# Performance work log

Measured on AMD Instinct MI355X. Metric: run time of the kernel, lower is better.

Reference implementation:

```python
import jax, jax.numpy as jnp
import numpy as np

TOP_K = 2


def setup_inputs() -> dict:
    key = jax.random.key(0)
    k1, k2, k3, k4 = jax.random.split(key, 4)
    B, S, H, I, E = 8, 2048, 768, 3072, 8
    x = jax.random.normal(k1, (B, S, H), dtype=jnp.float32)
    # kaiming_uniform-ish scale for weights
    router_w = jax.random.uniform(k2, (E, H), dtype=jnp.float32, minval=-1.0, maxval=1.0) * (1.0 / np.sqrt(H))
    up_w = jax.random.uniform(k3, (E, H, I), dtype=jnp.float32, minval=-1.0, maxval=1.0) * (1.0 / np.sqrt(H))
    down_w = jax.random.uniform(k4, (E, I, H), dtype=jnp.float32, minval=-1.0, maxval=1.0) * (1.0 / np.sqrt(I))
    return {"x": x, "router_w": router_w, "up_w": up_w, "down_w": down_w}


def reference(x, router_w, up_w, down_w):
    B, S, H = x.shape
    E = up_w.shape[0]
    T = B * S
    xf = x.reshape(T, H)
    # router: Linear(H -> E, bias=False) then softmax, top-k, renormalize
    logits = xf @ router_w.T                      # [T, E]
    probs = jax.nn.softmax(logits, axis=-1)
    top_w, top_i = jax.lax.top_k(probs, TOP_K)    # [T, K]
    top_w = top_w / jnp.sum(top_w, axis=-1, keepdims=True)
    # dense per-(token, expert) gate: zero for unselected experts
    gate = jnp.zeros((T, E), dtype=xf.dtype).at[jnp.arange(T)[:, None], top_i].add(top_w)
    # combine: sum_e gate[:, e] * down_e(gelu(up_e(x)))
    out = jnp.zeros_like(xf)
    for e in range(E):  # fixed small expert count; loop is structural, not over data dims
        h = jax.nn.gelu(xf @ up_w[e], approximate=False)   # exact GELU == torch F.gelu
        out = out + gate[:, e:e + 1] * (h @ down_w[e])
    return out.reshape(B, S, H)
```

## Files before the change

### kernel.cpp

```cpp
#include <hip/hip_runtime.h>

typedef short bf16x8 __attribute__((ext_vector_type(8)));
typedef float f32x4  __attribute__((ext_vector_type(4)));

#define T_TOK 16384
#define HD 768
#define ID 3072
#define NE 8

__device__ __forceinline__ unsigned short f2bf(float f) {
    unsigned int u = __float_as_uint(f);
    unsigned int r = (u + 0x7FFFu + ((u >> 16) & 1u)) >> 16;
    return (unsigned short)r;
}

__device__ __forceinline__ void gload16(const void* g, void* l) {
    __builtin_amdgcn_global_load_lds(
        (const __attribute__((address_space(1))) void*)g,
        (__attribute__((address_space(3))) void*)l, 16, 0, 0);
}

__global__ __launch_bounds__(256) void k_cvt_x(const float* __restrict__ x,
                                               unsigned short* __restrict__ xb) {
    int i = blockIdx.x * 256 + threadIdx.x;
    float4 v = ((const float4*)x)[i];
    ushort4 o;
    o.x = f2bf(v.x); o.y = f2bf(v.y); o.z = f2bf(v.z); o.w = f2bf(v.w);
    ((ushort4*)xb)[i] = o;
}

__global__ __launch_bounds__(256) void k_tp(const float* __restrict__ in,
                                            unsigned short* __restrict__ out,
                                            int R, int C) {
    __shared__ float t[64][65];
    const float* ine = in + (size_t)blockIdx.z * R * C;
    unsigned short* oute = out + (size_t)blockIdx.z * R * C;
    int c0 = blockIdx.x * 64, r0 = blockIdx.y * 64;
    int lc = threadIdx.x & 63, lr4 = threadIdx.x >> 6;
#pragma unroll
    for (int i = 0; i < 16; i++) {
        int r = i * 4 + lr4;
        t[r][lc] = ine[(size_t)(r0 + r) * C + c0 + lc];
    }
    __syncthreads();
#pragma unroll
    for (int i = 0; i < 16; i++) {
        int r = i * 4 + lr4;
        oute[(size_t)(c0 + r) * R + r0 + lc] = f2bf(t[lc][r]);
    }
}

__global__ __launch_bounds__(256) void k_router(const float* __restrict__ x,
                                                const float* __restrict__ rw,
                                                int* __restrict__ topE,
                                                float* __restrict__ topW) {
    __shared__ float lrw[NE * HD];
    for (int i = threadIdx.x; i < NE * HD; i += 256) lrw[i] = rw[i];
    __syncthreads();
    int lane = threadIdx.x & 63;
    int t = blockIdx.x * 4 + (threadIdx.x >> 6);
    const float* xr = x + (size_t)t * HD;
    float acc[NE] = {0, 0, 0, 0, 0, 0, 0, 0};
    for (int h = lane; h < HD; h += 64) {
        float xv = xr[h];
#pragma unroll
        for (int e = 0; e < NE; e++) acc[e] = fmaf(xv, lrw[e * HD + h], acc[e]);
    }
#pragma unroll
    for (int e = 0; e < NE; e++) {
        float v = acc[e];
#pragma unroll
        for (int o = 32; o > 0; o >>= 1) v += __shfl_xor(v, o, 64);
        acc[e] = v;
    }
    if (lane == 0) {
        int e1 = 0; float l1 = acc[0];
#pragma unroll
        for (int e = 1; e < NE; e++) if (acc[e] > l1) { l1 = acc[e]; e1 = e; }
        int e2 = -1; float l2 = -1e30f;
#pragma unroll
        for (int e = 0; e < NE; e++) if (e != e1 && acc[e] > l2) { l2 = acc[e]; e2 = e; }
        float ex = expf(l2 - l1);
        float w1 = 1.0f / (1.0f + ex);
        topE[2 * t] = e1; topE[2 * t + 1] = e2;
        topW[2 * t] = w1; topW[2 * t + 1] = ex * w1;
    }
}

__global__ __launch_bounds__(256) void k_scatter(const int* __restrict__ topE,
                                                 const float* __restrict__ topW,
                                                 int* __restrict__ counts,
                                                 int* __restrict__ tokL,
                                                 float* __restrict__ gateL) {
    __shared__ int lc[NE], lbase[NE];
    if (threadIdx.x < NE) lc[threadIdx.x] = 0;
    __syncthreads();
    int t = blockIdx.x * 256 + threadIdx.x;
    int e1 = topE[2 * t], e2 = topE[2 * t + 1];
    int p1 = atomicAdd(&lc[e1], 1);
    int p2 = atomicAdd(&lc[e2], 1);
    __syncthreads();
    if (threadIdx.x < NE) lbase[threadIdx.x] = atomicAdd(&counts[threadIdx.x], lc[threadIdx.x]);
    __syncthreads();
    int q1 = lbase[e1] + p1, q2 = lbase[e2] + p2;
    tokL[e1 * T_TOK + q1] = t;  gateL[e1 * T_TOK + q1] = topW[2 * t];
    tokL[e2 * T_TOK + q2] = t;  gateL[e2 * T_TOK + q2] = topW[2 * t + 1];
}

__global__ __launch_bounds__(512, 2) void k_moe(
    const unsigned short* __restrict__ xb,
    const unsigned short* __restrict__ upt,
    const unsigned short* __restrict__ dnt,
    const int* __restrict__ counts,
    const int* __restrict__ tokL,
    const float* __restrict__ gateL,
    float* __restrict__ out) {
    __shared__ __align__(16) char lds[155648];
    char* xs = lds;
    char* hs = lds + 98304;
    char* ring = lds + 106496;

    const int e = blockIdx.x & 7;
    const int slot = blockIdx.x >> 3;
    const int cnt = counts[e];
    if (slot * 64 >= cnt) return;
    const int nrow = min(64, cnt - slot * 64);
    const int* tok = tokL + e * T_TOK + slot * 64;
    const float* gat = gateL + e * T_TOK + slot * 64;

    const int tid = threadIdx.x;
    const int lane = tid & 63;
    const int wid = tid >> 6;
    const int mi = wid >> 2, ni = wid & 3;

    const char* upe = (const char*)(upt + (size_t)e * ID * HD);
    const char* dne = (const char*)(dnt + (size_t)e * HD * ID);

    {
        int off = tid * 16;
#pragma unroll
        for (int s = 0; s < 12; s++) {
            int o = off + s * 8192;
            int m = o / 1536;
            int cb = o - m * 1536;
            int tk = (m < nrow) ? tok[m] : tok[0];
            const char* src = (const char*)xb + (size_t)tk * 1536 + (size_t)(cb ^ ((m & 7) << 4));
            gload16(src, xs + s * 8192 + wid * 1024);
        }
    }
    asm volatile("s_waitcnt vmcnt(0)" ::: "memory");
    __builtin_amdgcn_s_barrier();
    asm volatile("" ::: "memory");

    auto issue = [&](int s) {
        char* dst = ring + (s % 6) * 8192 + wid * 1024;
        int ci = s / 24;
        int ph = s - ci * 24;
        int row = tid >> 3;
        int cb = (tid & 7) << 4;
        int scb = cb ^ ((row & 7) << 4);
        const char* src;
        if (ci >= 48) src = upe;
        else if (ph < 12) src = upe + (size_t)(ci * 64 + row) * 1536 + ph * 128 + scb;
        else              src = dne + (size_t)((ph - 12) * 64 + row) * 6144 + ci * 128 + scb;
        gload16(src, dst);
    };

    f32x4 acc[2][12];
#pragma unroll
    for (int a = 0; a < 2; a++)
#pragma unroll
        for (int b = 0; b < 12; b++) acc[a][b] = (f32x4){0.f, 0.f, 0.f, 0.f};

    issue(0); issue(1); issue(2); issue(3);

    f32x4 acch[2];
    bf16x8 ha[2][2];

    for (int ci = 0; ci < 48; ci++) {
#pragma unroll
        for (int ks = 0; ks < 12; ks++) {
            issue(ci * 24 + ks + 4);
            asm volatile("s_waitcnt vmcnt(4)" ::: "memory");
            __builtin_amdgcn_s_barrier();
            asm volatile("" ::: "memory");
            char* buf = ring + (ks % 6) * 8192;
            if (ks == 0) { acch[0] = (f32x4){0.f,0.f,0.f,0.f}; acch[1] = (f32x4){0.f,0.f,0.f,0.f}; }
#pragma unroll
            for (int kr = 0; kr < 2; kr++) {
                int bn = ni * 16 + (lane & 15);
                int bo = ((kr * 32 + (lane >> 4) * 8) * 2) ^ ((bn & 7) << 4);
                bf16x8 bfrag = *(const bf16x8*)(buf + bn * 128 + bo);
#pragma unroll
                for (int mr = 0; mr < 2; mr++) {
                    int ar = mi * 32 + mr * 16 + (lane & 15);
                    int ao = ((ks * 64 + kr * 32 + (lane >> 4) * 8) * 2) ^ ((ar & 7) << 4);
                    bf16x8 afrag = *(const bf16x8*)(xs + ar * 1536 + ao);
                    acch[mr] = __builtin_amdgcn_mfma_f32_16x16x32_bf16(afrag, bfrag, acch[mr], 0, 0, 0);
                }
            }
            if (ks == 11) {
#pragma unroll
                for (int mr = 0; mr < 2; mr++) {
                    int col = ni * 16 + (lane & 15);
#pragma unroll
                    for (int r = 0; r < 4; r++) {
                        int m = mi * 32 + mr * 16 + (lane >> 4) * 4 + r;
                        float v = acch[mr][r];
                        float g = 0.5f * v * (1.0f + erff(v * 0.70710678118f));
                        *(unsigned short*)(hs + m * 128 + ((col * 2) ^ ((m & 7) << 4))) = f2bf(g);
                    }
                }
                asm volatile("s_waitcnt lgkmcnt(0)" ::: "memory");
            }
        }
#pragma unroll
        for (int j = 0; j < 12; j++) {
            issue(ci * 24 + 12 + j + 4);
            asm volatile("s_waitcnt vmcnt(4)" ::: "memory");
            __builtin_amdgcn_s_barrier();
            asm volatile("" ::: "memory");
            char* buf = ring + ((12 + j) % 6) * 8192;
            if (j == 0) {
#pragma unroll
                for (int mr = 0; mr < 2; mr++)
#pragma unroll
                    for (int kr = 0; kr < 2; kr++) {
                        int ar = mi * 32 + mr * 16 + (lane & 15);
                        int ao = ((kr * 32 + (lane >> 4) * 8) * 2) ^ ((ar & 7) << 4);
                        ha[mr][kr] = *(const bf16x8*)(hs + ar * 128 + ao);
                    }
            }
#pragma unroll
            for (int kr = 0; kr < 2; kr++) {
                int bn = ni * 16 + (lane & 15);
                int bo = ((kr * 32 + (lane >> 4) * 8) * 2) ^ ((bn & 7) << 4);
                bf16x8 bfrag = *(const bf16x8*)(buf + bn * 128 + bo);
#pragma unroll
                for (int mr = 0; mr < 2; mr++)
                    acc[mr][j] = __builtin_amdgcn_mfma_f32_16x16x32_bf16(ha[mr][kr], bfrag, acc[mr][j], 0, 0, 0);
            }
        }
    }

    int   t4[2][4];
    float g4[2][4];
#pragma unroll
    for (int mr = 0; mr < 2; mr++)
#pragma unroll
        for (int r = 0; r < 4; r++) {
            int m = mi * 32 + mr * 16 + (lane >> 4) * 4 + r;
            bool valid = m < nrow;
            t4[mr][r] = valid ? tok[m] : -1;
            g4[mr][r] = valid ? gat[m] : 0.f;
        }
#pragma unroll
    for (int mr = 0; mr < 2; mr++)
#pragma unroll
        for (int j = 0; j < 12; j++) {
            int colg = j * 64 + ni * 16 + (lane & 15);
#pragma unroll
            for (int r = 0; r < 4; r++) {
                if (t4[mr][r] >= 0)
                    atomicAdd(out + (size_t)t4[mr][r] * HD + colg, g4[mr][r] * acc[mr][j][r]);
            }
        }
}

extern "C" void kernel_launch(void* const* d_in, const int* in_sizes, int n_in,
                              void* d_out, int out_size, void* d_ws, size_t ws_size,
                              hipStream_t stream) {
    const float* x  = (const float*)d_in[0];
    const float* rw = (const float*)d_in[1];
    const float* uw = (const float*)d_in[2];
    const float* dw = (const float*)d_in[3];
    float* out = (float*)d_out;

    char* w = (char*)d_ws;
    unsigned short* xb  = (unsigned short*)w; w += (size_t)T_TOK * HD * 2;
    unsigned short* upt = (unsigned short*)w; w += (size_t)NE * ID * HD * 2;
    unsigned short* dnt = (unsigned short*)w; w += (size_t)NE * HD * ID * 2;
    int*   topE   = (int*)w;   w += (size_t)T_TOK * 2 * 4;
    float* topW   = (float*)w; w += (size_t)T_TOK * 2 * 4;
    int*   counts = (int*)w;   w += 256;
    int*   tokL   = (int*)w;   w += (size_t)NE * T_TOK * 4;
    float* gateL  = (float*)w; w += (size_t)NE * T_TOK * 4;

    hipMemsetAsync(d_out, 0, (size_t)T_TOK * HD * 4, stream);
    hipMemsetAsync(counts, 0, 256, stream);

    k_cvt_x<<<(T_TOK * HD) / (256 * 4), 256, 0, stream>>>(x, xb);
    k_tp<<<dim3(ID / 64, HD / 64, NE), 256, 0, stream>>>(uw, upt, HD, ID);
    k_tp<<<dim3(HD / 64, ID / 64, NE), 256, 0, stream>>>(dw, dnt, ID, HD);
    k_router<<<T_TOK / 4, 256, 0, stream>>>(x, rw, topE, topW);
    k_scatter<<<T_TOK / 256, 256, 0, stream>>>(topE, topW, counts, tokL, gateL);
    k_moe<<<2048, 512, 0, stream>>>(xb, upt, dnt, counts, tokL, gateL, out);
}
```

Baseline: 779.4 us.

## Rewrite fused MoE kernel with compact tile list, register-held X and wider intermediate chunks

Replaces the MoE kernel with a new fused version. A small descriptor kernel builds a compact list of (expert, row-offset) tiles so no empty blocks are launched, and an XCD-aware swizzle maps blocks to tiles. The token activations are now held in registers instead of LDS. The intermediate dimension is processed in 128-wide chunks, with a 3-slot ring for up-projection weights and double-buffered down-projection slices. The up-projection and the down-projection loads are interleaved, and s_setprio is raised around MFMA bursts. Exact erff is swapped for a polynomial erf approximation. The 24 f32x4 down accumulators plus 24 held activation fragments raise register pressure, and the polynomial slightly changes GELU accuracy.

```diff
diff --git a/kernel.cpp b/kernel.cpp
--- a/kernel.cpp
+++ b/kernel.cpp
@@ -7,6 +7,7 @@
 #define HD 768
 #define ID 3072
 #define NE 8
+#define NTM64 520
 
 __device__ __forceinline__ unsigned short f2bf(float f) {
     unsigned int u = __float_as_uint(f);
@@ -18,6 +19,29 @@
     __builtin_amdgcn_global_load_lds(
         (const __attribute__((address_space(1))) void*)g,
         (__attribute__((address_space(3))) void*)l, 16, 0, 0);
+}
+
+__device__ __forceinline__ void vmw(int n) {
+    if (n == 0)      asm volatile("s_waitcnt vmcnt(0)" ::: "memory");
+    else if (n == 2) asm volatile("s_waitcnt vmcnt(2)" ::: "memory");
+    else if (n == 3) asm volatile("s_waitcnt vmcnt(3)" ::: "memory");
+    else             asm volatile("s_waitcnt vmcnt(4)" ::: "memory");
+}
+
+__device__ __forceinline__ float gelu_f(float x) {
+    float z = fabsf(x) * 0.70710678118f;
+    float t = 1.0f / fmaf(0.3275911f, z, 1.0f);
+    float p = t * fmaf(t, fmaf(t, fmaf(t, fmaf(t, 1.061405429f, -1.453152027f),
+                                       1.421413741f), -0.284496736f), 0.254829592f);
+    float e = 1.0f - p * __expf(-z * z);
+    float erfv = (x >= 0.f) ? e : -e;
+    return 0.5f * x * (1.0f + erfv);
+}
+
+__device__ __forceinline__ int xcd_swz(int bid, int nwg) {
+    int q = nwg >> 3, rr = nwg & 7;
+    int xcd = bid & 7, seq = bid >> 3;
+    return (xcd < rr ? xcd * (q + 1) : rr * (q + 1) + (xcd - rr) * q) + seq;
 }
 
 __global__ __launch_bounds__(256) void k_cvt_x(const float* __restrict__ x,
@@ -107,164 +131,181 @@
     tokL[e2 * T_TOK + q2] = t;  gateL[e2 * T_TOK + q2] = topW[2 * t + 1];
 }
 
-__global__ __launch_bounds__(512, 2) void k_moe(
+__global__ void k_desc(const int* __restrict__ counts, int* __restrict__ tileE,
+                       int* __restrict__ tileM0) {
+    if (threadIdx.x == 0 && blockIdx.x == 0) {
+        int tl = 0;
+        for (int e = 0; e < NE; e++) {
+            int c = counts[e];
+            int nt = (c + 63) >> 6;
+            for (int t = 0; t < nt; t++) { tileE[tl] = e; tileM0[tl] = t << 6; tl++; }
+        }
+        for (; tl < NTM64; tl++) { tileE[tl] = -1; tileM0[tl] = 0; }
+    }
+}
+
+__global__ __launch_bounds__(512, 2) void k_fused(
     const unsigned short* __restrict__ xb,
     const unsigned short* __restrict__ upt,
     const unsigned short* __restrict__ dnt,
     const int* __restrict__ counts,
     const int* __restrict__ tokL,
     const float* __restrict__ gateL,
+    const int* __restrict__ tileE,
+    const int* __restrict__ tileM0,
     float* __restrict__ out) {
-    __shared__ __align__(16) char lds[155648];
-    char* xs = lds;
-    char* hs = lds + 98304;
-    char* ring = lds + 106496;
-
-    const int e = blockIdx.x & 7;
-    const int slot = blockIdx.x >> 3;
-    const int cnt = counts[e];
-    if (slot * 64 >= cnt) return;
-    const int nrow = min(64, cnt - slot * 64);
-    const int* tok = tokL + e * T_TOK + slot * 64;
-    const float* gat = gateL + e * T_TOK + slot * 64;
-
-    const int tid = threadIdx.x;
-    const int lane = tid & 63;
-    const int wid = tid >> 6;
-    const int mi = wid >> 2, ni = wid & 3;
+    __shared__ __align__(16) char lds[163840];
+
+    int L = xcd_swz(blockIdx.x, gridDim.x);
+    int e = tileE[L];
+    if (e < 0) return;
+    int m0 = tileM0[L];
+    int nrow = min(64, counts[e] - m0);
+    const int* tok = tokL + e * T_TOK + m0;
+    const float* gat = gateL + e * T_TOK + m0;
+
+    const int tid = threadIdx.x, lane = tid & 63, wid = tid >> 6;
+    const int wm = wid >> 1, wn = wid & 1;
+    const int g = lane >> 4, r = lane & 15;
+    const int foff = g * 256 + r * 16;
 
     const char* upe = (const char*)(upt + (size_t)e * ID * HD);
-    const char* dne = (const char*)(dnt + (size_t)e * HD * ID);
-
+    const char* dne = (const char*)(dnt + (size_t)e * ID * HD);
+
+    bf16x8 xf[24];
     {
-        int off = tid * 16;
-#pragma unroll
-        for (int s = 0; s < 12; s++) {
-            int o = off + s * 8192;
-            int m = o / 1536;
-            int cb = o - m * 1536;
-            int tk = (m < nrow) ? tok[m] : tok[0];
-            const char* src = (const char*)xb + (size_t)tk * 1536 + (size_t)(cb ^ ((m & 7) << 4));
-            gload16(src, xs + s * 8192 + wid * 1024);
-        }
-    }
+        int row = wm * 16 + r;
+        int tk = tok[row < nrow ? row : 0];
+        const char* xs = (const char*)xb + (size_t)tk * 1536 + g * 16;
+#pragma unroll
+        for (int s = 0; s < 24; s++) xf[s] = *(const bf16x8*)(xs + s * 64);
+    }
+    int t4[4]; float g4[4];
+#pragma unroll
+    for (int j = 0; j < 4; j++) {
+        int rl = wm * 16 + g * 4 + j;
+        bool v = rl < nrow;
+        t4[j] = v ? tok[rl] : -1;
+        g4[j] = v ? gat[rl] : 0.f;
+    }
+
+    const char* uB = upe + (size_t)(wid * 16 + r) * 1536 + g * 16;
+    const char* dB0 = dne + (size_t)(wid * 96 + r) * 6144 + g * 16;
+
+    auto stgU = [&](int ci_, int t_, int slot_) {
+        const char* s0 = uB + (size_t)ci_ * 196608 + t_ * 128;
+        char* d = lds + 16384 + slot_ * 16384 + wid * 2048;
+        gload16(s0, d);
+        gload16(s0 + 64, d + 1024);
+    };
+
+    f32x4 accD[24];
+#pragma unroll
+    for (int n = 0; n < 24; n++) accD[n] = (f32x4){0.f, 0.f, 0.f, 0.f};
+
+    auto downStep = [&](const char* dsl, int s) {
+        bf16x8 af = *(const bf16x8*)(lds + (wm * 4 + s) * 1024 + foff);
+        __builtin_amdgcn_s_setprio(1);
+#pragma unroll
+        for (int grp = 0; grp < 4; grp++) {
+            bf16x8 bb[6];
+#pragma unroll
+            for (int q = 0; q < 6; q++)
+                bb[q] = *(const bf16x8*)(dsl + (wn * 24 + grp * 6 + q) * 1024 + foff);
+#pragma unroll
+            for (int q = 0; q < 6; q++)
+                accD[grp * 6 + q] = __builtin_amdgcn_mfma_f32_16x16x32_bf16(af, bb[q], accD[grp * 6 + q], 0, 0, 0);
+        }
+        __builtin_amdgcn_s_setprio(0);
+    };
+
+    stgU(0, 0, 0);
+    stgU(0, 1, 1);
     asm volatile("s_waitcnt vmcnt(0)" ::: "memory");
     __builtin_amdgcn_s_barrier();
     asm volatile("" ::: "memory");
 
-    auto issue = [&](int s) {
-        char* dst = ring + (s % 6) * 8192 + wid * 1024;
-        int ci = s / 24;
-        int ph = s - ci * 24;
-        int row = tid >> 3;
-        int cb = (tid & 7) << 4;
-        int scb = cb ^ ((row & 7) << 4);
-        const char* src;
-        if (ci >= 48) src = upe;
-        else if (ph < 12) src = upe + (size_t)(ci * 64 + row) * 1536 + ph * 128 + scb;
-        else              src = dne + (size_t)((ph - 12) * 64 + row) * 6144 + ci * 128 + scb;
-        gload16(src, dst);
-    };
-
-    f32x4 acc[2][12];
-#pragma unroll
-    for (int a = 0; a < 2; a++)
-#pragma unroll
-        for (int b = 0; b < 12; b++) acc[a][b] = (f32x4){0.f, 0.f, 0.f, 0.f};
-
-    issue(0); issue(1); issue(2); issue(3);
-
-    f32x4 acch[2];
-    bf16x8 ha[2][2];
-
-    for (int ci = 0; ci < 48; ci++) {
-#pragma unroll
-        for (int ks = 0; ks < 12; ks++) {
-            issue(ci * 24 + ks + 4);
-            asm volatile("s_waitcnt vmcnt(4)" ::: "memory");
+    for (int ci = 0; ci < 24; ci++) {
+        f32x4 ah[4];
+#pragma unroll
+        for (int n = 0; n < 4; n++) ah[n] = (f32x4){0.f, 0.f, 0.f, 0.f};
+
+#pragma unroll
+        for (int t = 0; t < 12; t++) {
+            if (t < 10) stgU(ci, t + 2, (t + 2) % 3);
+            {
+                int q = (t < 6) ? t : t - 6;
+                int ks = (t < 6) ? 0 : 1;
+                gload16(dB0 + (size_t)q * 98304 + ci * 256 + ks * 64,
+                        lds + 65536 + ks * 49152 + (wid * 6 + q) * 1024);
+            }
+            const char* ub = lds + 16384 + (t % 3) * 16384;
+            __builtin_amdgcn_s_setprio(1);
+#pragma unroll
+            for (int nf = 0; nf < 4; nf++)
+#pragma unroll
+                for (int kh = 0; kh < 2; kh++) {
+                    bf16x8 bb = *(const bf16x8*)(ub + ((wn * 4 + nf) * 2 + kh) * 1024 + foff);
+                    ah[nf] = __builtin_amdgcn_mfma_f32_16x16x32_bf16(xf[t * 2 + kh], bb, ah[nf], 0, 0, 0);
+                }
+            __builtin_amdgcn_s_setprio(0);
+            vmw((t == 0) ? 3 : (t <= 9) ? 4 : (t == 10) ? 2 : 0);
             __builtin_amdgcn_s_barrier();
             asm volatile("" ::: "memory");
-            char* buf = ring + (ks % 6) * 8192;
-            if (ks == 0) { acch[0] = (f32x4){0.f,0.f,0.f,0.f}; acch[1] = (f32x4){0.f,0.f,0.f,0.f}; }
-#pragma unroll
-            for (int kr = 0; kr < 2; kr++) {
-                int bn = ni * 16 + (lane & 15);
-                int bo = ((kr * 32 + (lane >> 4) * 8) * 2) ^ ((bn & 7) << 4);
-                bf16x8 bfrag = *(const bf16x8*)(buf + bn * 128 + bo);
-#pragma unroll
-                for (int mr = 0; mr < 2; mr++) {
-                    int ar = mi * 32 + mr * 16 + (lane & 15);
-                    int ao = ((ks * 64 + kr * 32 + (lane >> 4) * 8) * 2) ^ ((ar & 7) << 4);
-                    bf16x8 afrag = *(const bf16x8*)(xs + ar * 1536 + ao);
-                    acch[mr] = __builtin_amdgcn_mfma_f32_16x16x32_bf16(afrag, bfrag, acch[mr], 0, 0, 0);
-                }
+        }
+
+#pragma unroll
+        for (int nf = 0; nf < 4; nf++) {
+            int i = wn * 64 + nf * 16 + r;
+            int kk = i & 31, ks = i >> 5;
+#pragma unroll
+            for (int j = 0; j < 4; j++) {
+                int row = g * 4 + j;
+                *(unsigned short*)(lds + (wm * 4 + ks) * 1024 + (kk >> 3) * 256 + row * 16 + (kk & 7) * 2)
+                    = f2bf(gelu_f(ah[nf][j]));
             }
-            if (ks == 11) {
-#pragma unroll
-                for (int mr = 0; mr < 2; mr++) {
-                    int col = ni * 16 + (lane & 15);
-#pragma unroll
-                    for (int r = 0; r < 4; r++) {
-                        int m = mi * 32 + mr * 16 + (lane >> 4) * 4 + r;
-                        float v = acch[mr][r];
-                        float g = 0.5f * v * (1.0f + erff(v * 0.70710678118f));
-                        *(unsigned short*)(hs + m * 128 + ((col * 2) ^ ((m & 7) << 4))) = f2bf(g);
-                    }
-                }
-                asm volatile("s_waitcnt lgkmcnt(0)" ::: "memory");
-            }
-        }
-#pragma unroll
-        for (int j = 0; j < 12; j++) {
-            issue(ci * 24 + 12 + j + 4);
-            asm volatile("s_waitcnt vmcnt(4)" ::: "memory");
-            __builtin_amdgcn_s_barrier();
-            asm volatile("" ::: "memory");
-            char* buf = ring + ((12 + j) % 6) * 8192;
-            if (j == 0) {
-#pragma unroll
-                for (int mr = 0; mr < 2; mr++)
-#pragma unroll
-                    for (int kr = 0; kr < 2; kr++) {
-                        int ar = mi * 32 + mr * 16 + (lane & 15);
-                        int ao = ((kr * 32 + (lane >> 4) * 8) * 2) ^ ((ar & 7) << 4);
-                        ha[mr][kr] = *(const bf16x8*)(hs + ar * 128 + ao);
-                    }
-            }
-#pragma unroll
-            for (int kr = 0; kr < 2; kr++) {
-                int bn = ni * 16 + (lane & 15);
-                int bo = ((kr * 32 + (lane >> 4) * 8) * 2) ^ ((bn & 7) << 4);
-                bf16x8 bfrag = *(const bf16x8*)(buf + bn * 128 + bo);
-#pragma unroll
-                for (int mr = 0; mr < 2; mr++)
-                    acc[mr][j] = __builtin_amdgcn_mfma_f32_16x16x32_bf16(ha[mr][kr], bfrag, acc[mr][j], 0, 0, 0);
-            }
-        }
-    }
-
-    int   t4[2][4];
-    float g4[2][4];
-#pragma unroll
-    for (int mr = 0; mr < 2; mr++)
-#pragma unroll
-        for (int r = 0; r < 4; r++) {
-            int m = mi * 32 + mr * 16 + (lane >> 4) * 4 + r;
-            bool valid = m < nrow;
-            t4[mr][r] = valid ? tok[m] : -1;
-            g4[mr][r] = valid ? gat[m] : 0.f;
-        }
-#pragma unroll
-    for (int mr = 0; mr < 2; mr++)
-#pragma unroll
-        for (int j = 0; j < 12; j++) {
-            int colg = j * 64 + ni * 16 + (lane & 15);
-#pragma unroll
-            for (int r = 0; r < 4; r++) {
-                if (t4[mr][r] >= 0)
-                    atomicAdd(out + (size_t)t4[mr][r] * HD + colg, g4[mr][r] * acc[mr][j][r]);
-            }
-        }
+        }
+        asm volatile("s_waitcnt lgkmcnt(0)" ::: "memory");
+        __builtin_amdgcn_s_barrier();
+        asm volatile("" ::: "memory");
+
+        int cin = (ci + 1 < 24) ? ci + 1 : 23;
+        downStep(lds + 65536, 0);
+        __builtin_amdgcn_s_barrier();
+        asm volatile("" ::: "memory");
+#pragma unroll
+        for (int q = 0; q < 6; q++)
+            gload16(dB0 + (size_t)q * 98304 + ci * 256 + 2 * 64,
+                    lds + 65536 + (wid * 6 + q) * 1024);
+        stgU(cin, 0, 0);
+        downStep(lds + 65536 + 49152, 1);
+        vmw(2);
+        __builtin_amdgcn_s_barrier();
+        asm volatile("" ::: "memory");
+#pragma unroll
+        for (int q = 0; q < 6; q++)
+            gload16(dB0 + (size_t)q * 98304 + ci * 256 + 3 * 64,
+                    lds + 65536 + 49152 + (wid * 6 + q) * 1024);
+        stgU(cin, 1, 1);
+        downStep(lds + 65536, 2);
+        vmw(2);
+        __builtin_amdgcn_s_barrier();
+        asm volatile("" ::: "memory");
+        downStep(lds + 65536 + 49152, 3);
+        vmw(0);
+        __builtin_amdgcn_s_barrier();
+        asm volatile("" ::: "memory");
+    }
+
+#pragma unroll
+    for (int nf = 0; nf < 24; nf++) {
+        int col = wn * 384 + nf * 16 + r;
+#pragma unroll
+        for (int j = 0; j < 4; j++) {
+            if (t4[j] >= 0)
+                atomicAdd(out + (size_t)t4[j] * HD + col, g4[j] * accD[nf][j]);
+        }
+    }
 }
 
 extern "C" void kernel_launch(void* const* d_in, const int* in_sizes, int n_in,
@@ -276,15 +317,23 @@
     const float* dw = (const float*)d_in[3];
     float* out = (float*)d_out;
 
-    char* w = (char*)d_ws;
-    unsigned short* xb  = (unsigned short*)w; w += (size_t)T_TOK * HD * 2;
-    unsigned short* upt = (unsigned short*)w; w += (size_t)NE * ID * HD * 2;
-    unsigned short* dnt = (unsigned short*)w; w += (size_t)NE * HD * ID * 2;
-    int*   topE   = (int*)w;   w += (size_t)T_TOK * 2 * 4;
-    float* topW   = (float*)w; w += (size_t)T_TOK * 2 * 4;
-    int*   counts = (int*)w;   w += 256;
-    int*   tokL   = (int*)w;   w += (size_t)NE * T_TOK * 4;
-    float* gateL  = (float*)w; w += (size_t)NE * T_TOK * 4;
+    size_t off = 0;
+    char* base = (char*)d_ws;
+    auto alloc = [&](size_t bytes) -> char* {
+        char* p = base + off;
+        off += (bytes + 1023) & ~(size_t)1023;
+        return p;
+    };
+    unsigned short* xb   = (unsigned short*)alloc((size_t)T_TOK * HD * 2);
+    unsigned short* upt  = (unsigned short*)alloc((size_t)NE * ID * HD * 2);
+    unsigned short* dnt  = (unsigned short*)alloc((size_t)NE * HD * ID * 2);
+    int*   topE   = (int*)alloc((size_t)T_TOK * 2 * 4);
+    float* topW   = (float*)alloc((size_t)T_TOK * 2 * 4);
+    int*   counts = (int*)alloc(256);
+    int*   tileE  = (int*)alloc(NTM64 * 4);
+    int*   tileM0 = (int*)alloc(NTM64 * 4);
+    int*   tokL   = (int*)alloc((size_t)NE * T_TOK * 4);
+    float* gateL  = (float*)alloc((size_t)NE * T_TOK * 4);
 
     hipMemsetAsync(d_out, 0, (size_t)T_TOK * HD * 4, stream);
     hipMemsetAsync(counts, 0, 256, stream);
@@ -294,5 +343,6 @@
     k_tp<<<dim3(HD / 64, ID / 64, NE), 256, 0, stream>>>(dw, dnt, ID, HD);
     k_router<<<T_TOK / 4, 256, 0, stream>>>(x, rw, topE, topW);
     k_scatter<<<T_TOK / 256, 256, 0, stream>>>(topE, topW, counts, tokL, gateL);
-    k_moe<<<2048, 512, 0, stream>>>(xb, upt, dnt, counts, tokL, gateL, out);
-}
+    k_desc<<<1, 64, 0, stream>>>(counts, tileE, tileM0);
+    k_fused<<<NTM64, 512, 0, stream>>>(xb, upt, dnt, counts, tokL, gateL, tileE, tileM0, out);
+}
```

After: 1.176 ms. +50.8%, slower.
